# Kernel tuning notes

Hardware: AMD Instinct MI355X
Metric: run time of the kernel (lower is better)

The kernel has to match this reference:

```python
import jax, jax.numpy as jnp
import numpy as np

DIM = 768
NUM_HEADS = 12
HEAD_DIM = DIM // NUM_HEADS
B, N = 16, 784


def setup_inputs() -> dict:
    key = jax.random.key(0)
    k1, k2, k3, k4, k5 = jax.random.split(key, 5)
    x = jax.random.normal(k1, (B, N, DIM), dtype=jnp.float32)
    # Dense params (flax Dense: kernel [in, out], bias [out])
    Wqkv = jax.random.normal(k2, (DIM, 3 * DIM), dtype=jnp.float32) * (DIM ** -0.5)
    bqkv = jnp.zeros((3 * DIM,), dtype=jnp.float32)
    Wo = jax.random.normal(k3, (DIM, DIM), dtype=jnp.float32) * (DIM ** -0.5)
    bo = jnp.zeros((DIM,), dtype=jnp.float32)
    return {"x": x, "Wqkv": Wqkv, "bqkv": bqkv, "Wo": Wo, "bo": bo}


def reference(x, Wqkv, bqkv, Wo, bo):
    b, n, dim = x.shape
    # fused QKV projection
    qkv = jnp.einsum('bnd,df->bnf', x, Wqkv) + bqkv          # [b, n, 3*dim]
    qkv = qkv.reshape(b, n, 3, NUM_HEADS, HEAD_DIM)           # '(k h d)' split
    q, k, v = qkv[:, :, 0], qkv[:, :, 1], qkv[:, :, 2]        # [b, n, h, d]
    scale = HEAD_DIM ** -0.5
    # chunked/flash path computes exact softmax attention; same math, expressed densely
    scores = jnp.einsum('bihd,bjhd->bhij', q, k) * scale      # [b, h, n, n]
    attn = jax.nn.softmax(scores, axis=-1)
    out = jnp.einsum('bhij,bjhd->bihd', attn, v)              # [b, n, h, d]
    out = out.reshape(b, n, dim)                              # 'b n (h d)'
    return jnp.einsum('bnd,df->bnf', out, Wo) + bo
```

## Files before the change

kernel.cpp:

```cpp
#include <hip/hip_runtime.h>

#define DIM 768
#define NHEADS 12
#define HDIM 64
#define BB 16
#define NN 784
#define M_TOTAL (BB * NN)

typedef __attribute__((ext_vector_type(8))) _Float16 f16x8;
typedef __attribute__((ext_vector_type(4))) float f32x4;
typedef __attribute__((ext_vector_type(16))) float f32x16;
typedef __fp16 fp16x2 __attribute__((ext_vector_type(2)));

typedef __attribute__((address_space(3))) unsigned int lds_uint;
typedef __attribute__((address_space(1))) const unsigned int g_uint;
__device__ inline void gload_lds16(const void* g, void* l) {
    __builtin_amdgcn_global_load_lds((g_uint*)(uintptr_t)g,
                                     (lds_uint*)(uintptr_t)l, 16, 0, 0);
}

#if __has_builtin(__builtin_amdgcn_exp2f)
#define EXP2(x) __builtin_amdgcn_exp2f(x)
#else
#define EXP2(x) exp2f(x)
#endif

__device__ inline unsigned int pk2(float a, float b, float* lacc) {
#if __has_builtin(__builtin_amdgcn_cvt_pkrtz)
    union { fp16x2 h; unsigned int u; } r;
    r.h = __builtin_amdgcn_cvt_pkrtz(a, b);
#if __has_builtin(__builtin_amdgcn_fdot2)
    const fp16x2 one = {(__fp16)1.f, (__fp16)1.f};
    *lacc = __builtin_amdgcn_fdot2(r.h, one, *lacc, false);
#else
    *lacc += a + b;
#endif
    return r.u;
#else
    union { _Float16 h[2]; unsigned int u; } r;
    r.h[0] = (_Float16)a; r.h[1] = (_Float16)b;
    *lacc += a + b;
    return r.u;
#endif
}

__global__ __launch_bounds__(256) void cvt_f16_kernel(
    const float* __restrict__ in, _Float16* __restrict__ out, int n)
{
    int i = (blockIdx.x * 256 + threadIdx.x) * 8;
    if (i >= n) return;
    float4 a = *(const float4*)&in[i];
    float4 b = *(const float4*)&in[i + 4];
    union { _Float16 h[8]; uint4 v; } o;
    o.h[0] = (_Float16)a.x; o.h[1] = (_Float16)a.y;
    o.h[2] = (_Float16)a.z; o.h[3] = (_Float16)a.w;
    o.h[4] = (_Float16)b.x; o.h[5] = (_Float16)b.y;
    o.h[6] = (_Float16)b.z; o.h[7] = (_Float16)b.w;
    *(uint4*)&out[i] = o.v;
}

__global__ __launch_bounds__(256) void transpose_f16_kernel(
    const float* __restrict__ W, _Float16* __restrict__ T, int K, int N)
{
    __shared__ float t[32][33];
    const int n0 = blockIdx.x * 32, k0 = blockIdx.y * 32;
    const int r = threadIdx.x >> 3, c4 = (threadIdx.x & 7) * 4;
    float4 v = *(const float4*)&W[(size_t)(k0 + r) * N + n0 + c4];
    t[r][c4 + 0] = v.x; t[r][c4 + 1] = v.y;
    t[r][c4 + 2] = v.z; t[r][c4 + 3] = v.w;
    __syncthreads();
    union { _Float16 h[4]; ushort4 v4; } o;
#pragma unroll
    for (int i = 0; i < 4; ++i) o.h[i] = (_Float16)t[c4 + i][r];
    *(ushort4*)&T[(size_t)(n0 + r) * K + k0 + c4] = o.v4;
}

#define G_STAGE(BUF, K0)                                                       \
  {                                                                            \
    _Pragma("unroll")                                                          \
    for (int i = 0; i < 4; ++i) {                                              \
        const int rbase = w * 32 + i * 8;                                      \
        gload_lds16(A + (size_t)(gm + rbase + srow) * K + (K0) + scol,         \
                    &sA[BUF][rbase * 64]);                                     \
        gload_lds16(B + (size_t)(gn + rbase + srow) * K + (K0) + scol,         \
                    &sB[BUF][rbase * 64]);                                     \
    }                                                                          \
  }

#define G_COMPUTE(BUF)                                                         \
  {                                                                            \
    _Pragma("unroll")                                                          \
    for (int kk = 0; kk < 4; ++kk) {                                           \
        const int c = kk * 2 + hi;                                             \
        const int sw = (c ^ (l31 & 7)) * 8;                                    \
        f16x8 a[4], bb[2];                                                     \
        _Pragma("unroll")                                                      \
        for (int mt = 0; mt < 4; ++mt)                                         \
            a[mt] = *(const f16x8*)&sA[BUF][(wm + mt * 32 + l31) * 64 + sw];   \
        _Pragma("unroll")                                                      \
        for (int nt = 0; nt < 2; ++nt)                                         \
            bb[nt] = *(const f16x8*)&sB[BUF][(wn + nt * 32 + l31) * 64 + sw];  \
        __builtin_amdgcn_s_setprio(1);                                         \
        _Pragma("unroll")                                                      \
        for (int mt = 0; mt < 4; ++mt)                                         \
            _Pragma("unroll")                                                  \
            for (int nt = 0; nt < 2; ++nt)                                     \
                acc[mt][nt] = __builtin_amdgcn_mfma_f32_32x32x16_f16(          \
                    a[mt], bb[nt], acc[mt][nt], 0, 0, 0);                      \
        __builtin_amdgcn_s_setprio(0);                                         \
    }                                                                          \
  }

template <int OUT_F16>
__global__ __launch_bounds__(512) void gemm_f16_kernel(
    const _Float16* __restrict__ A, const _Float16* __restrict__ B,
    const float* __restrict__ bias, void* __restrict__ Cout,
    int M, int N, int K)
{
    __shared__ _Float16 sA[2][256 * 64];
    __shared__ _Float16 sB[2][256 * 64];

    const int tid  = threadIdx.x;
    const int w    = tid >> 6;
    const int lane = tid & 63;

    const int nwg = gridDim.x * gridDim.y;
    const int lid = blockIdx.x + gridDim.x * blockIdx.y;
    const int cq  = nwg >> 3, cr = nwg & 7;
    const int xcd = lid & 7, ix = lid >> 3;
    const int wgid = (xcd < cr ? xcd * (cq + 1) : cr * (cq + 1) + (xcd - cr) * cq) + ix;
    const int gn = (wgid % gridDim.x) * 256;
    const int gm = (wgid / gridDim.x) * 256;

    const int wm = (w & 1) * 128;
    const int wn = (w >> 1) * 64;
    const int l31 = lane & 31;
    const int hi  = lane >> 5;

    const int srow = lane >> 3;
    const int scol = ((lane & 7) ^ srow) * 8;

    f32x16 acc[4][2] = {};

    const int NT = K >> 6;
    G_STAGE(0, 0)
    __syncthreads();
    int cur = 0;
#pragma unroll 1
    for (int t = 0; t < NT - 1; ++t) {
        G_STAGE(cur ^ 1, (t + 1) * 64)
        G_COMPUTE(cur)
        __syncthreads();
        cur ^= 1;
    }
    G_COMPUTE(cur)

#pragma unroll
    for (int nt = 0; nt < 2; ++nt) {
        const int col = gn + wn + nt * 32 + l31;
        const float bv = bias[col];
#pragma unroll
        for (int mt = 0; mt < 4; ++mt) {
            f32x16 v = acc[mt][nt];
#pragma unroll
            for (int reg = 0; reg < 16; ++reg) {
                const int row = gm + wm + mt * 32 + (reg & 3) + 8 * (reg >> 2) + 4 * hi;
                const float o = v[reg] + bv;
                if (OUT_F16)
                    ((_Float16*)Cout)[(size_t)row * N + col] = (_Float16)o;
                else
                    ((float*)Cout)[(size_t)row * N + col] = o;
            }
        }
    }
}

#define LOG2E_8 0.18033688f

#define LOAD_TILE(J0, TAIL)                                                    \
  {                                                                            \
    const int j0_ = (J0);                                                      \
    int jrowK = j0_ + sj;                                                      \
    if (TAIL && jrowK > NN - 1) jrowK = NN - 1;                                \
    const size_t kbase = (size_t)(b * NN + jrowK) * (3 * DIM) + DIM + h * HDIM;\
    k0v = *(const uint4*)&qkv[kbase + sg * 8];                                 \
    k1v = *(const uint4*)&qkv[kbase + sg * 8 + 32];                            \
    int vr0 = j0_ + 2 * jj, vr1 = j0_ + 2 * jj + 1;                            \
    if (TAIL) { if (vr0 > NN - 1) vr0 = NN - 1; if (vr1 > NN - 1) vr1 = NN - 1; } \
    va.v = *(const uint4*)&qkv[(size_t)(b * NN + vr0) * (3 * DIM) + 2 * DIM + h * HDIM + dsub]; \
    vc.v = *(const uint4*)&qkv[(size_t)(b * NN + vr1) * (3 * DIM) + 2 * DIM + h * HDIM + dsub]; \
  }

#define WRITE_TILE(BUF)                                                        \
  {                                                                            \
    _Float16 (*K_)[72] = Ks[BUF];                                              \
    _Float16 (*V_)[72] = Vt[BUF];                                              \
    *(uint4*)&K_[sj][sg * 8]      = k0v;                                       \
    *(uint4*)&K_[sj][sg * 8 + 32] = k1v;                                       \
    _Pragma("unroll")                                                          \
    for (int i = 0; i < 8; ++i) {                                              \
        union { _Float16 h2[2]; unsigned int u; } t;                           \
        t.h2[0] = va.h[i]; t.h2[1] = vc.h[i];                                  \
        *(unsigned int*)&V_[dsub + i][pcol] = t.u;                             \
    }                                                                          \
  }

#define EXP_PACK(SV, G, J0_, TAIL)                                             \
  {                                                                            \
    float p0 = EXP2(SV[0]), p1 = EXP2(SV[1]);                                  \
    float p2 = EXP2(SV[2]), p3 = EXP2(SV[3]);                                  \
    if (TAIL && (J0_ + nt * 16) >= NN) { p0 = p1 = p2 = p3 = 0.f; }            \
    pk[G][nt][0] = pk2(p0, p1, &lpart[G]);                                     \
    pk[G][nt][1] = pk2(p2, p3, &lpart[G]);                                     \
  }

#define COMPUTE_TILE(BUF, J0, TAIL)                                            \
  {                                                                            \
    _Float16 (*K_)[72] = Ks[BUF];                                              \
    _Float16 (*V_)[72] = Vt[BUF];                                              \
    unsigned int pk[2][4][2];                                                  \
    _Pragma("unroll")                                                          \
    for (int nt = 0; nt < 4; ++nt) {                                           \
        f16x8 kf0 = *(const f16x8*)&K_[nt * 16 + l16][quad * 8];               \
        f16x8 kf1 = *(const f16x8*)&K_[nt * 16 + l16][32 + quad * 8];          \
        f32x4 s0 = {}, s1 = {};                                                \
        s0 = __builtin_amdgcn_mfma_f32_16x16x32_f16(kf0, qfrag[0][0], s0, 0, 0, 0); \
        s0 = __builtin_amdgcn_mfma_f32_16x16x32_f16(kf1, qfrag[0][1], s0, 0, 0, 0); \
        s1 = __builtin_amdgcn_mfma_f32_16x16x32_f16(kf0, qfrag[1][0], s1, 0, 0, 0); \
        s1 = __builtin_amdgcn_mfma_f32_16x16x32_f16(kf1, qfrag[1][1], s1, 0, 0, 0); \
        EXP_PACK(s0, 0, J0, TAIL)                                              \
        EXP_PACK(s1, 1, J0, TAIL)                                              \
    }                                                                          \
    __builtin_amdgcn_s_setprio(1);                                             \
    _Pragma("unroll")                                                          \
    for (int pc = 0; pc < 2; ++pc) {                                           \
        union { unsigned int u[4]; f16x8 v; } pa0, pa1;                        \
        pa0.u[0] = pk[0][2 * pc][0];     pa0.u[1] = pk[0][2 * pc][1];          \
        pa0.u[2] = pk[0][2 * pc + 1][0]; pa0.u[3] = pk[0][2 * pc + 1][1];      \
        pa1.u[0] = pk[1][2 * pc][0];     pa1.u[1] = pk[1][2 * pc][1];          \
        pa1.u[2] = pk[1][2 * pc + 1][0]; pa1.u[3] = pk[1][2 * pc + 1][1];      \
        _Pragma("unroll")                                                      \
        for (int dt = 0; dt < 4; ++dt) {                                       \
            f16x8 vf = *(const f16x8*)&V_[dt * 16 + l16][pc * 32 + quad * 8];  \
            O[0][dt] = __builtin_amdgcn_mfma_f32_16x16x32_f16(pa0.v, vf, O[0][dt], 0, 0, 0); \
            O[1][dt] = __builtin_amdgcn_mfma_f32_16x16x32_f16(pa1.v, vf, O[1][dt], 0, 0, 0); \
        }                                                                      \
    }                                                                          \
    __builtin_amdgcn_s_setprio(0);                                             \
  }

__global__ __launch_bounds__(256, 2) void attn_f16_kernel(
    const _Float16* __restrict__ qkv, _Float16* __restrict__ oat)
{
    const int L   = blockIdx.x + 7 * (blockIdx.y + NHEADS * blockIdx.z);
    const int xcd = L & 7, ixc = L >> 3;
    const int grp = xcd * 24 + ixc / 7;
    const int q0  = (ixc % 7) * 128;
    const int b   = grp / NHEADS;
    const int h   = grp % NHEADS;

    const int tid = threadIdx.x;
    const int wave = tid >> 6;
    const int lane = tid & 63;
    const int quad = lane >> 4;
    const int l16  = lane & 15;

    __shared__ _Float16 Ks[2][64][72];
    __shared__ _Float16 Vt[2][64][72];

    f16x8 qfrag[2][2];
#pragma unroll
    for (int g = 0; g < 2; ++g) {
        int qrow = q0 + wave * 32 + g * 16 + l16; if (qrow > NN - 1) qrow = NN - 1;
        size_t base = (size_t)(b * NN + qrow) * (3 * DIM) + h * HDIM;
        qfrag[g][0] = (*(const f16x8*)&qkv[base + quad * 8]) * (_Float16)LOG2E_8;
        qfrag[g][1] = (*(const f16x8*)&qkv[base + 32 + quad * 8]) * (_Float16)LOG2E_8;
    }

    const int sj = lane;
    const int sg = wave;
    const int jj   = lane & 31;
    const int dsub = sg * 16 + (lane >> 5) * 8;
    const int pcol = ((jj >> 4) << 5) | (((jj >> 1) & 3) << 3)
                   | (((jj >> 3) & 1) << 2) | ((jj & 1) << 1);

    f32x4 O[2][4] = {};
    float lpart[2] = {0.f, 0.f};

    uint4 k0v, k1v;
    union { uint4 v; _Float16 h[8]; } va, vc;

    LOAD_TILE(0, 0)
#pragma unroll 1
    for (int jt = 0; jt < 11; ++jt) {
        WRITE_TILE(jt & 1)
        __syncthreads();
        LOAD_TILE((jt + 1) * 64, 0)
        COMPUTE_TILE(jt & 1, 0, 0)
    }
    WRITE_TILE(1)
    __syncthreads();
    LOAD_TILE(768, 1)
    COMPUTE_TILE(1, 704, 0)
    WRITE_TILE(0)
    __syncthreads();
    COMPUTE_TILE(0, 768, 1)

#pragma unroll
    for (int g = 0; g < 2; ++g) {
        float t = lpart[g];
        t += __shfl_xor(t, 16);
        t += __shfl_xor(t, 32);
        float inv[4];
#pragma unroll
        for (int r = 0; r < 4; ++r)
            inv[r] = 1.0f / __shfl(t, quad * 4 + r, 16);
#pragma unroll
        for (int r = 0; r < 4; ++r) {
            const int q = q0 + wave * 32 + g * 16 + quad * 4 + r;
            if (q < NN) {
#pragma unroll
                for (int dt = 0; dt < 4; ++dt) {
                    const size_t base = (size_t)(b * NN + q) * DIM + h * HDIM + dt * 16 + l16;
                    oat[base] = (_Float16)(O[g][dt][r] * inv[r]);
                }
            }
        }
    }
}

extern "C" void kernel_launch(void* const* d_in, const int* in_sizes, int n_in,
                              void* d_out, int out_size, void* d_ws, size_t ws_size,
                              hipStream_t stream) {
    const float* x    = (const float*)d_in[0];
    const float* Wqkv = (const float*)d_in[1];
    const float* bqkv = (const float*)d_in[2];
    const float* Wo   = (const float*)d_in[3];
    const float* bo   = (const float*)d_in[4];
    float* out = (float*)d_out;

    _Float16* qkv = (_Float16*)d_ws;
    _Float16* xh  = qkv + (size_t)M_TOTAL * 3 * DIM;
    _Float16* wqT = xh + (size_t)M_TOTAL * DIM;
    _Float16* woT = wqT + (size_t)3 * DIM * DIM;
    _Float16* oat = xh;

    {
        int n = M_TOTAL * DIM;
        cvt_f16_kernel<<<n / 8 / 256, 256, 0, stream>>>(x, xh, n);
    }
    transpose_f16_kernel<<<dim3((3 * DIM) / 32, DIM / 32), 256, 0, stream>>>(
        Wqkv, wqT, DIM, 3 * DIM);
    transpose_f16_kernel<<<dim3(DIM / 32, DIM / 32), 256, 0, stream>>>(
        Wo, woT, DIM, DIM);
    gemm_f16_kernel<1><<<dim3((3 * DIM) / 256, M_TOTAL / 256), 512, 0, stream>>>(
        xh, wqT, bqkv, qkv, M_TOTAL, 3 * DIM, DIM);
    attn_f16_kernel<<<dim3(7, NHEADS, BB), 256, 0, stream>>>(qkv, oat);
    gemm_f16_kernel<0><<<dim3(DIM / 256, M_TOTAL / 256), 512, 0, stream>>>(
        oat, woT, bo, out, M_TOTAL, DIM, DIM);
}
```

Before: 232.8 us.

## Restructure GEMM into four-stage K=32 pipeline with split A/B prefetch

```diff
diff --git a/kernel.cpp b/kernel.cpp
--- a/kernel.cpp
+++ b/kernel.cpp
@@ -75,41 +75,21 @@
     *(ushort4*)&T[(size_t)(n0 + r) * K + k0 + c4] = o.v4;
 }
 
-#define G_STAGE(BUF, K0)                                                       \
-  {                                                                            \
-    _Pragma("unroll")                                                          \
-    for (int i = 0; i < 4; ++i) {                                              \
-        const int rbase = w * 32 + i * 8;                                      \
-        gload_lds16(A + (size_t)(gm + rbase + srow) * K + (K0) + scol,         \
-                    &sA[BUF][rbase * 64]);                                     \
-        gload_lds16(B + (size_t)(gn + rbase + srow) * K + (K0) + scol,         \
-                    &sB[BUF][rbase * 64]);                                     \
-    }                                                                          \
-  }
-
-#define G_COMPUTE(BUF)                                                         \
-  {                                                                            \
-    _Pragma("unroll")                                                          \
-    for (int kk = 0; kk < 4; ++kk) {                                           \
-        const int c = kk * 2 + hi;                                             \
-        const int sw = (c ^ (l31 & 7)) * 8;                                    \
-        f16x8 a[4], bb[2];                                                     \
-        _Pragma("unroll")                                                      \
-        for (int mt = 0; mt < 4; ++mt)                                         \
-            a[mt] = *(const f16x8*)&sA[BUF][(wm + mt * 32 + l31) * 64 + sw];   \
-        _Pragma("unroll")                                                      \
-        for (int nt = 0; nt < 2; ++nt)                                         \
-            bb[nt] = *(const f16x8*)&sB[BUF][(wn + nt * 32 + l31) * 64 + sw];  \
-        __builtin_amdgcn_s_setprio(1);                                         \
-        _Pragma("unroll")                                                      \
-        for (int mt = 0; mt < 4; ++mt)                                         \
-            _Pragma("unroll")                                                  \
-            for (int nt = 0; nt < 2; ++nt)                                     \
-                acc[mt][nt] = __builtin_amdgcn_mfma_f32_32x32x16_f16(          \
-                    a[mt], bb[nt], acc[mt][nt], 0, 0, 0);                      \
-        __builtin_amdgcn_s_setprio(0);                                         \
-    }                                                                          \
-  }
+#define VMCNT(N) asm volatile("s_waitcnt vmcnt(" #N ")" ::: "memory")
+#define BARRIER() { asm volatile("" ::: "memory"); \
+                    __builtin_amdgcn_s_barrier();  \
+                    asm volatile("" ::: "memory"); }
+
+#define STAGE_A2(Q, K0)                                                        \
+  { gload_lds16(A + (size_t)(gm + w * 32 + srow) * K + (K0) + gc8,             \
+                &sA[Q][(w * 32) * 32]);                                        \
+    gload_lds16(A + (size_t)(gm + w * 32 + 16 + srow) * K + (K0) + gc8,        \
+                &sA[Q][(w * 32 + 16) * 32]); }
+#define STAGE_B2(Q, K0)                                                        \
+  { gload_lds16(B + (size_t)(gn + w * 32 + srow) * K + (K0) + gc8,             \
+                &sB[Q][(w * 32) * 32]);                                        \
+    gload_lds16(B + (size_t)(gn + w * 32 + 16 + srow) * K + (K0) + gc8,        \
+                &sB[Q][(w * 32 + 16) * 32]); }
 
 template <int OUT_F16>
 __global__ __launch_bounds__(512) void gemm_f16_kernel(
@@ -117,8 +97,8 @@
     const float* __restrict__ bias, void* __restrict__ Cout,
     int M, int N, int K)
 {
-    __shared__ _Float16 sA[2][256 * 64];
-    __shared__ _Float16 sB[2][256 * 64];
+    __shared__ _Float16 sA[4][256 * 32];
+    __shared__ _Float16 sB[4][256 * 32];
 
     const int tid  = threadIdx.x;
     const int w    = tid >> 6;
@@ -137,23 +117,73 @@
     const int l31 = lane & 31;
     const int hi  = lane >> 5;
 
-    const int srow = lane >> 3;
-    const int scol = ((lane & 7) ^ srow) * 8;
+    const int srow = lane >> 2;
+    const int gc8  = (((lane & 3) ^ (srow & 3)) * 8);
 
     f32x16 acc[4][2] = {};
 
-    const int NT = K >> 6;
-    G_STAGE(0, 0)
-    __syncthreads();
-    int cur = 0;
+    const int NT = K >> 5;
+
+    STAGE_A2(0, 0) STAGE_B2(0, 0)
+    STAGE_A2(1, 32) STAGE_B2(1, 32)
+    VMCNT(4);
+    BARRIER();
+
 #pragma unroll 1
-    for (int t = 0; t < NT - 1; ++t) {
-        G_STAGE(cur ^ 1, (t + 1) * 64)
-        G_COMPUTE(cur)
-        __syncthreads();
-        cur ^= 1;
-    }
-    G_COMPUTE(cur)
+    for (int r = 0; r < NT; ++r) {
+        const int q  = r & 3;
+        const int qn = (r + 2) & 3;
+        const int kn = (r + 2) * 32;
+        const _Float16* __restrict__ sa = sA[q];
+        const _Float16* __restrict__ sb = sB[q];
+
+        {
+            const int p = (0 * 2 + hi) ^ (l31 & 3);
+            f16x8 a0 = *(const f16x8*)&sa[(wm +   0 + l31) * 32 + p * 8];
+            f16x8 a1 = *(const f16x8*)&sa[(wm +  32 + l31) * 32 + p * 8];
+            f16x8 a2 = *(const f16x8*)&sa[(wm +  64 + l31) * 32 + p * 8];
+            f16x8 a3 = *(const f16x8*)&sa[(wm +  96 + l31) * 32 + p * 8];
+            f16x8 b0 = *(const f16x8*)&sb[(wn +   0 + l31) * 32 + p * 8];
+            f16x8 b1 = *(const f16x8*)&sb[(wn +  32 + l31) * 32 + p * 8];
+            if (r + 2 < NT) STAGE_A2(qn, kn)
+            BARRIER();
+            __builtin_amdgcn_s_setprio(1);
+            acc[0][0] = __builtin_amdgcn_mfma_f32_32x32x16_f16(a0, b0, acc[0][0], 0, 0, 0);
+            acc[0][1] = __builtin_amdgcn_mfma_f32_32x32x16_f16(a0, b1, acc[0][1], 0, 0, 0);
+            acc[1][0] = __builtin_amdgcn_mfma_f32_32x32x16_f16(a1, b0, acc[1][0], 0, 0, 0);
+            acc[1][1] = __builtin_amdgcn_mfma_f32_32x32x16_f16(a1, b1, acc[1][1], 0, 0, 0);
+            acc[2][0] = __builtin_amdgcn_mfma_f32_32x32x16_f16(a2, b0, acc[2][0], 0, 0, 0);
+            acc[2][1] = __builtin_amdgcn_mfma_f32_32x32x16_f16(a2, b1, acc[2][1], 0, 0, 0);
+            acc[3][0] = __builtin_amdgcn_mfma_f32_32x32x16_f16(a3, b0, acc[3][0], 0, 0, 0);
+            acc[3][1] = __builtin_amdgcn_mfma_f32_32x32x16_f16(a3, b1, acc[3][1], 0, 0, 0);
+            __builtin_amdgcn_s_setprio(0);
+            BARRIER();
+        }
+        {
+            const int p = (1 * 2 + hi) ^ (l31 & 3);
+            f16x8 a0 = *(const f16x8*)&sa[(wm +   0 + l31) * 32 + p * 8];
+            f16x8 a1 = *(const f16x8*)&sa[(wm +  32 + l31) * 32 + p * 8];
+            f16x8 a2 = *(const f16x8*)&sa[(wm +  64 + l31) * 32 + p * 8];
+            f16x8 a3 = *(const f16x8*)&sa[(wm +  96 + l31) * 32 + p * 8];
+            f16x8 b0 = *(const f16x8*)&sb[(wn +   0 + l31) * 32 + p * 8];
+            f16x8 b1 = *(const f16x8*)&sb[(wn +  32 + l31) * 32 + p * 8];
+            if (r + 2 < NT) STAGE_B2(qn, kn)
+            BARRIER();
+            __builtin_amdgcn_s_setprio(1);
+            acc[0][0] = __builtin_amdgcn_mfma_f32_32x32x16_f16(a0, b0, acc[0][0], 0, 0, 0);
+            acc[0][1] = __builtin_amdgcn_mfma_f32_32x32x16_f16(a0, b1, acc[0][1], 0, 0, 0);
+            acc[1][0] = __builtin_amdgcn_mfma_f32_32x32x16_f16(a1, b0, acc[1][0], 0, 0, 0);
+            acc[1][1] = __builtin_amdgcn_mfma_f32_32x32x16_f16(a1, b1, acc[1][1], 0, 0, 0);
+            acc[2][0] = __builtin_amdgcn_mfma_f32_32x32x16_f16(a2, b0, acc[2][0], 0, 0, 0);
+            acc[2][1] = __builtin_amdgcn_mfma_f32_32x32x16_f16(a2, b1, acc[2][1], 0, 0, 0);
+            acc[3][0] = __builtin_amdgcn_mfma_f32_32x32x16_f16(a3, b0, acc[3][0], 0, 0, 0);
+            acc[3][1] = __builtin_amdgcn_mfma_f32_32x32x16_f16(a3, b1, acc[3][1], 0, 0, 0);
+            __builtin_amdgcn_s_setprio(0);
+            if (r + 2 < NT)      { VMCNT(4); }
+            else if (r + 1 < NT) { VMCNT(0); }
+            BARRIER();
+        }
+    }
 
 #pragma unroll
     for (int nt = 0; nt < 2; ++nt) {
```

Result: slower. 249.9 us (+7.4%).

## Stage GEMM epilogue through LDS for coalesced stores; merge prep kernels

Applied to the files above, without the earlier changes.

```diff
diff --git a/kernel.cpp b/kernel.cpp
--- a/kernel.cpp
+++ b/kernel.cpp
@@ -44,26 +44,42 @@
 #endif
 }
 
-__global__ __launch_bounds__(256) void cvt_f16_kernel(
-    const float* __restrict__ in, _Float16* __restrict__ out, int n)
+__global__ __launch_bounds__(256) void prep_kernel(
+    const float* __restrict__ x, _Float16* __restrict__ xh,
+    const float* __restrict__ Wqkv, _Float16* __restrict__ wqT,
+    const float* __restrict__ Wo, _Float16* __restrict__ woT)
 {
-    int i = (blockIdx.x * 256 + threadIdx.x) * 8;
-    if (i >= n) return;
-    float4 a = *(const float4*)&in[i];
-    float4 b = *(const float4*)&in[i + 4];
-    union { _Float16 h[8]; uint4 v; } o;
-    o.h[0] = (_Float16)a.x; o.h[1] = (_Float16)a.y;
-    o.h[2] = (_Float16)a.z; o.h[3] = (_Float16)a.w;
-    o.h[4] = (_Float16)b.x; o.h[5] = (_Float16)b.y;
-    o.h[6] = (_Float16)b.z; o.h[7] = (_Float16)b.w;
-    *(uint4*)&out[i] = o.v;
-}
-
-__global__ __launch_bounds__(256) void transpose_f16_kernel(
-    const float* __restrict__ W, _Float16* __restrict__ T, int K, int N)
-{
+    const int NC  = (M_TOTAL * DIM) / (8 * 256);
+    const int NQX = (3 * DIM) / 32;
+    const int NQ  = NQX * (DIM / 32);
+    const int NOX = DIM / 32;
+    const int bid = blockIdx.x;
+
+    if (bid < NC) {
+        const int i = (bid * 256 + threadIdx.x) * 8;
+        float4 a = *(const float4*)&x[i];
+        float4 b = *(const float4*)&x[i + 4];
+        union { _Float16 h[8]; uint4 v; } o;
+        o.h[0] = (_Float16)a.x; o.h[1] = (_Float16)a.y;
+        o.h[2] = (_Float16)a.z; o.h[3] = (_Float16)a.w;
+        o.h[4] = (_Float16)b.x; o.h[5] = (_Float16)b.y;
+        o.h[6] = (_Float16)b.z; o.h[7] = (_Float16)b.w;
+        *(uint4*)&xh[i] = o.v;
+        return;
+    }
+
     __shared__ float t[32][33];
-    const int n0 = blockIdx.x * 32, k0 = blockIdx.y * 32;
+    const float* W; _Float16* T; int N, n0, k0;
+    if (bid < NC + NQ) {
+        const int lb = bid - NC;
+        W = Wqkv; T = wqT; N = 3 * DIM;
+        n0 = (lb % NQX) * 32; k0 = (lb / NQX) * 32;
+    } else {
+        const int lb = bid - NC - NQ;
+        W = Wo; T = woT; N = DIM;
+        n0 = (lb % NOX) * 32; k0 = (lb / NOX) * 32;
+    }
+    const int K = DIM;
     const int r = threadIdx.x >> 3, c4 = (threadIdx.x & 7) * 4;
     float4 v = *(const float4*)&W[(size_t)(k0 + r) * N + n0 + c4];
     t[r][c4 + 0] = v.x; t[r][c4 + 1] = v.y;
@@ -75,15 +91,18 @@
     *(ushort4*)&T[(size_t)(n0 + r) * K + k0 + c4] = o.v4;
 }
 
+#define SA(B) (smem + (B) * 16384)
+#define SB(B) (smem + 32768 + (B) * 16384)
+
 #define G_STAGE(BUF, K0)                                                       \
   {                                                                            \
     _Pragma("unroll")                                                          \
     for (int i = 0; i < 4; ++i) {                                              \
         const int rbase = w * 32 + i * 8;                                      \
         gload_lds16(A + (size_t)(gm + rbase + srow) * K + (K0) + scol,         \
-                    &sA[BUF][rbase * 64]);                                     \
+                    SA(BUF) + rbase * 64);                                     \
         gload_lds16(B + (size_t)(gn + rbase + srow) * K + (K0) + scol,         \
-                    &sB[BUF][rbase * 64]);                                     \
+                    SB(BUF) + rbase * 64);                                     \
     }                                                                          \
   }
 
@@ -96,10 +115,10 @@
         f16x8 a[4], bb[2];                                                     \
         _Pragma("unroll")                                                      \
         for (int mt = 0; mt < 4; ++mt)                                         \
-            a[mt] = *(const f16x8*)&sA[BUF][(wm + mt * 32 + l31) * 64 + sw];   \
+            a[mt] = *(const f16x8*)(SA(BUF) + (wm + mt * 32 + l31) * 64 + sw); \
         _Pragma("unroll")                                                      \
         for (int nt = 0; nt < 2; ++nt)                                         \
-            bb[nt] = *(const f16x8*)&sB[BUF][(wn + nt * 32 + l31) * 64 + sw];  \
+            bb[nt] = *(const f16x8*)(SB(BUF) + (wn + nt * 32 + l31) * 64 + sw);\
         __builtin_amdgcn_s_setprio(1);                                         \
         _Pragma("unroll")                                                      \
         for (int mt = 0; mt < 4; ++mt)                                         \
@@ -117,8 +136,7 @@
     const float* __restrict__ bias, void* __restrict__ Cout,
     int M, int N, int K)
 {
-    __shared__ _Float16 sA[2][256 * 64];
-    __shared__ _Float16 sB[2][256 * 64];
+    __shared__ _Float16 smem[4 * 256 * 64];
 
     const int tid  = threadIdx.x;
     const int w    = tid >> 6;
@@ -154,24 +172,65 @@
         cur ^= 1;
     }
     G_COMPUTE(cur)
-
-#pragma unroll
-    for (int nt = 0; nt < 2; ++nt) {
-        const int col = gn + wn + nt * 32 + l31;
-        const float bv = bias[col];
-#pragma unroll
-        for (int mt = 0; mt < 4; ++mt) {
-            f32x16 v = acc[mt][nt];
-#pragma unroll
-            for (int reg = 0; reg < 16; ++reg) {
-                const int row = gm + wm + mt * 32 + (reg & 3) + 8 * (reg >> 2) + 4 * hi;
-                const float o = v[reg] + bv;
-                if (OUT_F16)
-                    ((_Float16*)Cout)[(size_t)row * N + col] = (_Float16)o;
-                else
-                    ((float*)Cout)[(size_t)row * N + col] = o;
+    __syncthreads();
+
+#pragma unroll 1
+    for (int q = 0; q < 4; ++q) {
+        if ((w >> 1) == q) {
+            if (OUT_F16) {
+                _Float16* eb = (_Float16*)smem;
+#pragma unroll
+                for (int nt = 0; nt < 2; ++nt) {
+                    const float bv = bias[gn + q * 64 + nt * 32 + l31];
+#pragma unroll
+                    for (int mt = 0; mt < 4; ++mt) {
+                        f32x16 v = acc[mt][nt];
+#pragma unroll
+                        for (int reg = 0; reg < 16; ++reg) {
+                            const int row = wm + mt * 32 + (reg & 3) + 8 * (reg >> 2) + 4 * hi;
+                            eb[row * 72 + nt * 32 + l31] = (_Float16)(v[reg] + bv);
+                        }
+                    }
+                }
+            } else {
+                float* eb = (float*)smem;
+#pragma unroll
+                for (int nt = 0; nt < 2; ++nt) {
+                    const float bv = bias[gn + q * 64 + nt * 32 + l31];
+#pragma unroll
+                    for (int mt = 0; mt < 4; ++mt) {
+                        f32x16 v = acc[mt][nt];
+#pragma unroll
+                        for (int reg = 0; reg < 16; ++reg) {
+                            const int row = wm + mt * 32 + (reg & 3) + 8 * (reg >> 2) + 4 * hi;
+                            eb[row * 72 + nt * 32 + l31] = v[reg] + bv;
+                        }
+                    }
+                }
             }
         }
+        __syncthreads();
+        {
+            const int row = tid >> 1, seg = tid & 1;
+            if (OUT_F16) {
+                const _Float16* eb = (const _Float16*)smem;
+                _Float16* cp = (_Float16*)Cout + (size_t)(gm + row) * N
+                             + gn + q * 64 + seg * 32;
+                const _Float16* sp = eb + row * 72 + seg * 32;
+#pragma unroll
+                for (int k = 0; k < 4; ++k)
+                    *(uint4*)(cp + k * 8) = *(const uint4*)(sp + k * 8);
+            } else {
+                const float* eb = (const float*)smem;
+                float* cp = (float*)Cout + (size_t)(gm + row) * N
+                          + gn + q * 64 + seg * 32;
+                const float* sp = eb + row * 72 + seg * 32;
+#pragma unroll
+                for (int k = 0; k < 8; ++k)
+                    *(uint4*)(cp + k * 4) = *(const uint4*)(sp + k * 4);
+            }
+        }
+        __syncthreads();
     }
 }
 
@@ -346,13 +405,12 @@
     _Float16* oat = xh;
 
     {
-        int n = M_TOTAL * DIM;
-        cvt_f16_kernel<<<n / 8 / 256, 256, 0, stream>>>(x, xh, n);
-    }
-    transpose_f16_kernel<<<dim3((3 * DIM) / 32, DIM / 32), 256, 0, stream>>>(
-        Wqkv, wqT, DIM, 3 * DIM);
-    transpose_f16_kernel<<<dim3(DIM / 32, DIM / 32), 256, 0, stream>>>(
-        Wo, woT, DIM, DIM);
+        const int NC = (M_TOTAL * DIM) / (8 * 256);
+        const int NQ = ((3 * DIM) / 32) * (DIM / 32);
+        const int NO_ = (DIM / 32) * (DIM / 32);
+        prep_kernel<<<NC + NQ + NO_, 256, 0, stream>>>(
+            x, xh, Wqkv, wqT, Wo, woT);
+    }
     gemm_f16_kernel<1><<<dim3((3 * DIM) / 256, M_TOTAL / 256), 512, 0, stream>>>(
         xh, wqT, bqkv, qkv, M_TOTAL, 3 * DIM, DIM);
     attn_f16_kernel<<<dim3(7, NHEADS, BB), 256, 0, stream>>>(qkv, oat);
```

New measurement: 258.5 us. +11.1%, slower.
